# Performance work log

Measured on AMD Instinct MI355X. Metric: run time of the kernel, lower is better.

## Reference

```python
import jax, jax.numpy as jnp
import numpy as np

B, S, D, H = 2, 2048, 1024, 16
DK = D // H  # 64


def setup_inputs() -> dict:
    key = jax.random.key(0)
    ks = jax.random.split(key, 8)
    q = jax.random.normal(ks[0], (B, S, D), dtype=jnp.float32)
    k = jax.random.normal(ks[1], (B, S, D), dtype=jnp.float32)
    v = jax.random.normal(ks[2], (B, S, D), dtype=jnp.float32)
    mask = jax.random.randint(ks[3], (B, 1, S, S), 0, 2, dtype=jnp.int32)
    scale = 1.0 / np.sqrt(D)
    Wq = jax.random.normal(ks[4], (D, D), dtype=jnp.float32) * scale
    Wk = jax.random.normal(ks[5], (D, D), dtype=jnp.float32) * scale
    Wv = jax.random.normal(ks[6], (D, D), dtype=jnp.float32) * scale
    Wo = jax.random.normal(ks[7], (D, D), dtype=jnp.float32) * scale
    return {"q": q, "k": k, "v": v, "mask": mask,
            "Wq": Wq, "Wk": Wk, "Wv": Wv, "Wo": Wo}


def reference(q, k, v, mask, Wq, Wk, Wv, Wo):
    # Linear projections (torch nn.Linear: x @ W.T, no bias)
    qh = (q @ Wq.T).reshape(B, S, H, DK).transpose(0, 2, 1, 3)  # [B,H,S,DK]
    kh = (k @ Wk.T).reshape(B, S, H, DK).transpose(0, 2, 1, 3)
    vh = (v @ Wv.T).reshape(B, S, H, DK).transpose(0, 2, 1, 3)
    # Scaled dot-product attention with mask fill of -1e9 where mask == 0
    scores = jnp.einsum('bhqd,bhkd->bhqk', qh, kh) / jnp.sqrt(jnp.float32(DK))
    scores = jnp.where(mask == 0, jnp.float32(-1e9), scores)
    attn = jax.nn.softmax(scores, axis=-1)
    ctx = jnp.einsum('bhqk,bhkd->bhqd', attn, vh)  # [B,H,S,DK]
    ctx = ctx.transpose(0, 2, 1, 3).reshape(B, S, D)
    return ctx @ Wo.T
```

## Files before the change

### kernel.cpp

```cpp
#include <hip/hip_runtime.h>

using u16    = unsigned short;
using u32    = unsigned int;
using f32x4  = __attribute__((ext_vector_type(4))) float;
using f32x16 = __attribute__((ext_vector_type(16))) float;
using bf16x8 = __attribute__((ext_vector_type(8))) __bf16;
using u16x4  = __attribute__((ext_vector_type(4))) u16;
using u16x8  = __attribute__((ext_vector_type(8))) u16;
using u32x2  = __attribute__((ext_vector_type(2))) u32;
using u32x4  = __attribute__((ext_vector_type(4))) u32;
using i32x4  = __attribute__((ext_vector_type(4))) int;


__device__ __forceinline__ u16 f2bf(float f) {
  union { __bf16 b; u16 u; } c; c.b = (__bf16)f; return c.u;
}

typedef __attribute__((address_space(1))) const void GVoid;
typedef __attribute__((address_space(3))) void LVoid;

__device__ __forceinline__ void gload_lds16(const void* g, void* l) {
  __builtin_amdgcn_global_load_lds((GVoid*)g, (LVoid*)l, 16, 0, 0);
}

__global__ void cvt_w(const float* __restrict__ a, const float* __restrict__ b,
                      const float* __restrict__ c, const float* __restrict__ dd,
                      u16* __restrict__ oa, u16* __restrict__ ob,
                      u16* __restrict__ oc, u16* __restrict__ od) {
  int y = blockIdx.y;
  const float* s = (y == 0) ? a : (y == 1) ? b : (y == 2) ? c : dd;
  u16* d = (y == 0) ? oa : (y == 1) ? ob : (y == 2) ? oc : od;
  int i = blockIdx.x * 256 + threadIdx.x;
  f32x4 v = ((const f32x4*)s)[i];
  u16x4 r;
#pragma unroll
  for (int j = 0; j < 4; ++j) r[j] = f2bf(v[j]);
  ((u16x4*)d)[i] = r;
}

__global__ void pack_mask(const int* __restrict__ m, u32* __restrict__ mp) {
  int tid = blockIdx.x * 256 + threadIdx.x;
  int q = tid & 2047, kt = (tid >> 11) & 31, b = tid >> 16;
  const i32x4* src = (const i32x4*)(m + ((size_t)(b * 2048 + q)) * 2048 + kt * 64);
  u32 w0 = 0, w1 = 0;
#pragma unroll
  for (int j = 0; j < 8; ++j) {
    i32x4 a = src[j], c = src[j + 8];
#pragma unroll
    for (int e = 0; e < 4; ++e) {
      w0 |= (a[e] != 0 ? 1u : 0u) << (j * 4 + e);
      w1 |= (c[e] != 0 ? 1u : 0u) << (j * 4 + e);
    }
  }
  ((u32x2*)mp)[((size_t)(b * 32 + kt)) * 2048 + q] = u32x2{w0, w1};
}

__global__ __launch_bounds__(256, 2) void gemm_qkv(const float* __restrict__ Aq,
                                                   const float* __restrict__ Ak,
                                                   const float* __restrict__ Av,
                                                   const u16* __restrict__ Wb,
                                                   u16* __restrict__ out) {
  __shared__ alignas(16) char lds[32768];
  const int t = threadIdx.x;
  const int lane = t & 63, wid = t >> 6;
  const int g = lane >> 4, r16 = lane & 15;
  const int wm = wid >> 1, wn = wid & 1;
  const int m0 = blockIdx.x * 128, n0 = blockIdx.y * 128;
  const int z = blockIdx.z;

  const float* Axf = (z == 0) ? Aq : (z == 1) ? Ak : Av;
  const char* Ab = (const char*)Axf;
  const char* Bb = (const char*)(Wb + (size_t)z * 1048576);
  u16* op = out + (size_t)z * 4194304;
  const float qsc = (z == 0) ? 0.18033688011f : 1.0f;

  f32x4 acc[4][4] = {};

  for (int kk = 0; kk < 1024; kk += 64) {
#pragma unroll
    for (int i = 0; i < 4; ++i) {
      int ci = i * 256 + t;
      int row = ci >> 3;
      int cbs = ((ci & 7) << 4) ^ ((row & 7) << 4);
      gload_lds16(Bb + (size_t)(n0 + row) * 2048 + kk * 2 + cbs, lds + 16384 + ci * 16);
    }
#pragma unroll
    for (int i = 0; i < 4; ++i) {
      int ci = i * 256 + t;
      int row = ci >> 3;
      int cbs = ((ci & 7) << 4) ^ ((row & 7) << 4);
      const char* src = Ab + (size_t)(m0 + row) * 4096 + kk * 4 + cbs * 2;
      f32x4 a0 = *(const f32x4*)(src);
      f32x4 a1 = *(const f32x4*)(src + 16);
      u16x8 pk;
#pragma unroll
      for (int j = 0; j < 4; ++j) { pk[j] = f2bf(a0[j]); pk[4 + j] = f2bf(a1[j]); }
      *(u16x8*)(lds + ci * 16) = pk;
    }
    __syncthreads();
#pragma unroll
    for (int kc = 0; kc < 2; ++kc) {
      bf16x8 af[4], bfr[4];
#pragma unroll
      for (int mf = 0; mf < 4; ++mf) {
        int row = wm * 64 + mf * 16 + r16;
        af[mf] = *(const bf16x8*)(lds + row * 128 + ((64 * kc + 16 * g) ^ ((row & 7) << 4)));
      }
#pragma unroll
      for (int nf = 0; nf < 4; ++nf) {
        int row = wn * 64 + nf * 16 + r16;
        bfr[nf] = *(const bf16x8*)(lds + 16384 + row * 128 + ((64 * kc + 16 * g) ^ ((row & 7) << 4)));
      }
#pragma unroll
      for (int mf = 0; mf < 4; ++mf)
#pragma unroll
        for (int nf = 0; nf < 4; ++nf)
          acc[mf][nf] = __builtin_amdgcn_mfma_f32_16x16x32_bf16(af[mf], bfr[nf], acc[mf][nf], 0, 0, 0);
    }
    __syncthreads();
  }

#pragma unroll
  for (int mf = 0; mf < 4; ++mf) {
#pragma unroll
    for (int nf = 0; nf < 4; ++nf) {
      int mb = m0 + wm * 64 + mf * 16 + 4 * g;
      int n = n0 + wn * 64 + nf * 16 + r16;
      if (z == 0) {
        int bb = mb >> 11, h = n >> 6, dk = n & 63;
#pragma unroll
        for (int r = 0; r < 4; ++r) {
          int s = (mb + r) & 2047;
          op[((size_t)(bb * 16 + h) * 2048 + s) * 64 + dk] = f2bf(acc[mf][nf][r] * qsc);
        }
      } else if (z == 1) {
        int h = n >> 6, dk = n & 63;
#pragma unroll
        for (int r = 0; r < 4; ++r) {
          int m = mb + r;
          int bb = m >> 11, s = m & 2047;
          size_t off16 = ((((size_t)(bb * 16 + h) * 32 + (s >> 6)) * 2 + ((s >> 5) & 1)) * 8 +
                          (dk >> 3)) * 32 + (s & 31);
          op[off16 * 8 + (dk & 7)] = f2bf(acc[mf][nf][r]);
        }
      } else {
        int bb = mb >> 11, s = mb & 2047, h = n >> 6, d = n & 63;
        size_t off16 = ((((size_t)(bb * 16 + h) * 32 + (s >> 6)) * 8 + ((s & 63) >> 3)) * 2 +
                        (d >> 5)) * 32 + (d & 31);
        u16x4 pv;
#pragma unroll
        for (int r = 0; r < 4; ++r) pv[r] = f2bf(acc[mf][nf][r]);
        *(u16x4*)(op + off16 * 8 + (s & 7)) = pv;
      }
    }
  }
}

__global__ __launch_bounds__(256, 2) void gemm_out(const u16* __restrict__ X,
                                                   const u16* __restrict__ W,
                                                   float* __restrict__ out) {
  __shared__ alignas(16) char lds[32768];
  const int t = threadIdx.x;
  const int lane = t & 63, wid = t >> 6;
  const int g = lane >> 4, r16 = lane & 15;
  const int wm = wid >> 1, wn = wid & 1;
  const int m0 = blockIdx.x * 128, n0 = blockIdx.y * 128;
  const char* Ab = (const char*)X;
  const char* Bb = (const char*)W;

  f32x4 acc[4][4] = {};

  for (int kk = 0; kk < 1024; kk += 64) {
#pragma unroll
    for (int i = 0; i < 4; ++i) {
      int ci = i * 256 + t;
      int row = ci >> 3;
      int cbs = ((ci & 7) << 4) ^ ((row & 7) << 4);
      gload_lds16(Ab + (size_t)(m0 + row) * 2048 + kk * 2 + cbs, lds + ci * 16);
      gload_lds16(Bb + (size_t)(n0 + row) * 2048 + kk * 2 + cbs, lds + 16384 + ci * 16);
    }
    __syncthreads();
#pragma unroll
    for (int kc = 0; kc < 2; ++kc) {
      bf16x8 af[4], bfr[4];
#pragma unroll
      for (int mf = 0; mf < 4; ++mf) {
        int row = wm * 64 + mf * 16 + r16;
        af[mf] = *(const bf16x8*)(lds + row * 128 + ((64 * kc + 16 * g) ^ ((row & 7) << 4)));
      }
#pragma unroll
      for (int nf = 0; nf < 4; ++nf) {
        int row = wn * 64 + nf * 16 + r16;
        bfr[nf] = *(const bf16x8*)(lds + 16384 + row * 128 + ((64 * kc + 16 * g) ^ ((row & 7) << 4)));
      }
#pragma unroll
      for (int mf = 0; mf < 4; ++mf)
#pragma unroll
        for (int nf = 0; nf < 4; ++nf)
          acc[mf][nf] = __builtin_amdgcn_mfma_f32_16x16x32_bf16(af[mf], bfr[nf], acc[mf][nf], 0, 0, 0);
    }
    __syncthreads();
  }

#pragma unroll
  for (int mf = 0; mf < 4; ++mf)
#pragma unroll
    for (int nf = 0; nf < 4; ++nf) {
      int mb = m0 + wm * 64 + mf * 16 + 4 * g;
      int n = n0 + wn * 64 + nf * 16 + r16;
#pragma unroll
      for (int r = 0; r < 4; ++r) out[(size_t)(mb + r) * 1024 + n] = acc[mf][nf][r];
    }
}

struct KF { bf16x8 k0[4], k1[4]; };

__device__ __forceinline__ void loadK(KF& f, const char* p) {
#pragma unroll
  for (int c = 0; c < 4; ++c) {
    f.k0[c] = *(const bf16x8*)(p + c * 1024);
    f.k1[c] = *(const bf16x8*)(p + 4096 + c * 1024);
  }
}

__device__ __forceinline__ void attn_body(const bf16x8 (&qf)[4], KF& cur, KF& nxt,
                                          const char*& kp, const char*& vp0,
                                          const char*& vp1, const u32x2*& mptr,
                                          u32x2& mcur, int hi,
                                          f32x16& o0, f32x16& o1, float& l_run) {
  bf16x8 v0[4], v1[4];
#pragma unroll
  for (int ks = 0; ks < 4; ++ks) {
    v0[ks] = *(const bf16x8*)(vp0 + ks * 2048);
    v1[ks] = *(const bf16x8*)(vp1 + ks * 2048);
  }
  loadK(nxt, kp);
  u32x2 mnext = *mptr;
  kp += 8192; vp0 += 8192; vp1 += 8192; mptr += 2048;
  __builtin_amdgcn_sched_barrier(0);

  f32x16 s0 = {}, s1 = {};
#pragma unroll
  for (int c = 0; c < 4; ++c) {
    s0 = __builtin_amdgcn_mfma_f32_32x32x16_bf16(cur.k0[c], qf[c], s0, 0, 0, 0);
    s1 = __builtin_amdgcn_mfma_f32_32x32x16_bf16(cur.k1[c], qf[c], s1, 0, 0, 0);
  }

  u32 wa = mcur.x >> (4 * hi), wb = mcur.y >> (4 * hi);
  float ps = 0.f;
#pragma unroll
  for (int r = 0; r < 16; ++r) {
    const int bit = (r & 3) + 8 * (r >> 2);
    float p0 = __builtin_amdgcn_exp2f(s0[r]);
    float p1 = __builtin_amdgcn_exp2f(s1[r]);
    int sm0 = ((int)(wa << (31 - bit))) >> 31;
    int sm1 = ((int)(wb << (31 - bit))) >> 31;
    p0 = __uint_as_float(__float_as_uint(p0) & (u32)sm0);
    p1 = __uint_as_float(__float_as_uint(p1) & (u32)sm1);
    s0[r] = p0; s1[r] = p1;
    ps += p0 + p1;
  }
  l_run += ps;

  u32 w[16];
#pragma unroll
  for (int kb = 0; kb < 2; ++kb) {
#pragma unroll
    for (int ss = 0; ss < 2; ++ss) {
      const f32x16& sp = kb ? s1 : s0;
      u32 A0, B0, A1, B1;
      asm("v_cvt_pk_bf16_f32 %0, %1, %2" : "=v"(A0) : "v"(sp[8*ss+0]), "v"(sp[8*ss+1]));
      asm("v_cvt_pk_bf16_f32 %0, %1, %2" : "=v"(B0) : "v"(sp[8*ss+2]), "v"(sp[8*ss+3]));
      asm("v_cvt_pk_bf16_f32 %0, %1, %2" : "=v"(A1) : "v"(sp[8*ss+4]), "v"(sp[8*ss+5]));
      asm("v_cvt_pk_bf16_f32 %0, %1, %2" : "=v"(B1) : "v"(sp[8*ss+6]), "v"(sp[8*ss+7]));
      asm("v_permlane32_swap_b32 %0, %1" : "+v"(A0), "+v"(A1));
      asm("v_permlane32_swap_b32 %0, %1" : "+v"(B0), "+v"(B1));
      int f = 2 * kb + ss;
      w[4*f+0] = A0; w[4*f+1] = B0; w[4*f+2] = A1; w[4*f+3] = B1;
    }
  }

#pragma unroll
  for (int ks = 0; ks < 4; ++ks) {
    bf16x8 pa = __builtin_bit_cast(bf16x8, u32x4{w[4*ks], w[4*ks+1], w[4*ks+2], w[4*ks+3]});
    o0 = __builtin_amdgcn_mfma_f32_32x32x16_bf16(pa, v0[ks], o0, 0, 0, 0);
    o1 = __builtin_amdgcn_mfma_f32_32x32x16_bf16(pa, v1[ks], o1, 0, 0, 0);
  }
  mcur = mnext;
}

__global__ __launch_bounds__(256, 2) void attn_kern(const u16* __restrict__ Qh,
                                                    const u16* __restrict__ Kh,
                                                    const u16* __restrict__ Vt,
                                                    const u32* __restrict__ mp,
                                                    u16* __restrict__ ctx) {
  __shared__ float cmb[2][32][64];
  __shared__ float cmbl[2][64];
  const int t = threadIdx.x;
  const int wid = t >> 6, lane = t & 63;
  const int qw = wid & 1, kh = wid >> 1;
  const int hi = lane >> 5, l31 = lane & 31;

  const int wg = (blockIdx.x & 7) * 128 + (blockIdx.x >> 3);
  const int qt = wg & 31, bh = wg >> 5;
  const int b = bh >> 4, h = bh & 15;

  const char* qbytes = (const char*)Qh;
  const int qbase = qt * 64 + qw * 32;
  const int qg = qbase + l31;

  bf16x8 qf[4];
#pragma unroll
  for (int c = 0; c < 4; ++c)
    qf[c] = *(const bf16x8*)(qbytes + ((size_t)bh * 2048 + qg) * 128 + 32 * c + 16 * hi);

  const char* kp  = (const char*)Kh + (size_t)bh * 262144 + (size_t)kh * 131072 + hi * 512 + l31 * 16;
  const char* vp0 = (const char*)Vt + (size_t)bh * 262144 + (size_t)kh * 131072 + hi * 1024 + l31 * 16;
  const char* vp1 = vp0 + 512;
  const u32x2* mptr = (const u32x2*)mp + (size_t)b * 65536 + (size_t)kh * 32768 + qg;

  f32x16 o0 = {}, o1 = {};
  float l_run = 0.f;

  KF A, B2;
  loadK(A, kp);
  kp += 8192;
  u32x2 mcur = *mptr;
  mptr += 2048;

#pragma unroll 1
  for (int it = 0; it < 8; ++it) {
    attn_body(qf, A, B2, kp, vp0, vp1, mptr, mcur, hi, o0, o1, l_run);
    attn_body(qf, B2, A, kp, vp0, vp1, mptr, mcur, hi, o0, o1, l_run);
  }

  l_run += __shfl_xor(l_run, 32, 64);

  if (kh) {
#pragma unroll
    for (int r = 0; r < 16; ++r) {
      cmb[qw][r][lane]      = o0[r];
      cmb[qw][16 + r][lane] = o1[r];
    }
    cmbl[qw][lane] = l_run;
  }
  __syncthreads();
  if (!kh) {
#pragma unroll
    for (int r = 0; r < 16; ++r) {
      o0[r] += cmb[qw][r][lane];
      o1[r] += cmb[qw][16 + r][lane];
    }
    l_run += cmbl[qw][lane];

    float rl = 1.f / l_run;
#pragma unroll
    for (int r = 0; r < 16; ++r) {
      float rv = __shfl(rl, (r & 3) + 8 * (r >> 2) + 4 * hi, 64);
      int q = qbase + (r & 3) + 8 * (r >> 2) + 4 * hi;
      size_t rowp = ((size_t)b * 2048 + q) * 1024 + h * 64 + l31;
      ctx[rowp]      = f2bf(o0[r] * rv);
      ctx[rowp + 32] = f2bf(o1[r] * rv);
    }
  }
}

extern "C" void kernel_launch(void* const* d_in, const int* in_sizes, int n_in,
                              void* d_out, int out_size, void* d_ws, size_t ws_size,
                              hipStream_t stream) {
  const float* q  = (const float*)d_in[0];
  const float* k  = (const float*)d_in[1];
  const float* v  = (const float*)d_in[2];
  const int* mask = (const int*)d_in[3];
  const float* Wq = (const float*)d_in[4];
  const float* Wk = (const float*)d_in[5];
  const float* Wv = (const float*)d_in[6];
  const float* Wo = (const float*)d_in[7];

  u16* ws = (u16*)d_ws;
  const size_t NX = (size_t)4096 * 1024;
  const size_t NW = (size_t)1024 * 1024;
  u16* Wqb = ws + 3 * NX;
  u16* Qh  = Wqb + 4 * NW;
  u16* ctx = Qh + 3 * NX;
  u32* mpk = (u32*)ws;

  cvt_w<<<dim3(1024, 4), 256, 0, stream>>>(Wq, Wk, Wv, Wo,
                                           Wqb, Wqb + NW, Wqb + 2 * NW, Wqb + 3 * NW);
  pack_mask<<<dim3(512), 256, 0, stream>>>(mask, mpk);
  gemm_qkv<<<dim3(32, 8, 3), 256, 0, stream>>>(q, k, v, Wqb, Qh);
  attn_kern<<<dim3(1024), 256, 0, stream>>>(Qh, Qh + NX, Qh + 2 * NX, mpk, ctx);
  gemm_out<<<dim3(32, 8), 256, 0, stream>>>(ctx, Wqb + 3 * NW, (float*)d_out);
}
```

Measured before the change: 132.7 us.

## Prefetch next fp32 A tile into registers during QKV projection GEMM

The QKV projection GEMM now issues the fp32 activation loads for the next K-step into registers before the current step's MFMA work, using a two-buffer ping-pong loop unrolled by two. __syncthreads is replaced with explicit s_waitcnt vmcnt(8) plus raw s_barrier, so the prefetched loads stay in flight while the B tile's global_load_lds completes. The aim is to hide global-memory latency for the A operand. In exchange it uses more registers (32 extra f32x4), and the hand-counted vmcnt has to match the real number of outstanding loads.

```diff
diff --git a/kernel.cpp b/kernel.cpp
--- a/kernel.cpp
+++ b/kernel.cpp
@@ -76,7 +76,20 @@
 
   f32x4 acc[4][4] = {};
 
-  for (int kk = 0; kk < 1024; kk += 64) {
+  auto loadA = [&](f32x4 (&d0)[4], f32x4 (&d1)[4], int kk) {
+#pragma unroll
+    for (int i = 0; i < 4; ++i) {
+      int ci = i * 256 + t;
+      int row = ci >> 3;
+      int cbs = ((ci & 7) << 4) ^ ((row & 7) << 4);
+      const char* src = Ab + (size_t)(m0 + row) * 4096 + kk * 4 + cbs * 2;
+      d0[i] = *(const f32x4*)(src);
+      d1[i] = *(const f32x4*)(src + 16);
+    }
+  };
+
+  auto body = [&](int kk, f32x4 (&c0)[4], f32x4 (&c1)[4],
+                  f32x4 (&nn0)[4], f32x4 (&nn1)[4], bool pre) {
 #pragma unroll
     for (int i = 0; i < 4; ++i) {
       int ci = i * 256 + t;
@@ -87,17 +100,19 @@
 #pragma unroll
     for (int i = 0; i < 4; ++i) {
       int ci = i * 256 + t;
-      int row = ci >> 3;
-      int cbs = ((ci & 7) << 4) ^ ((row & 7) << 4);
-      const char* src = Ab + (size_t)(m0 + row) * 4096 + kk * 4 + cbs * 2;
-      f32x4 a0 = *(const f32x4*)(src);
-      f32x4 a1 = *(const f32x4*)(src + 16);
       u16x8 pk;
 #pragma unroll
-      for (int j = 0; j < 4; ++j) { pk[j] = f2bf(a0[j]); pk[4 + j] = f2bf(a1[j]); }
+      for (int j = 0; j < 4; ++j) { pk[j] = f2bf(c0[i][j]); pk[4 + j] = f2bf(c1[i][j]); }
       *(u16x8*)(lds + ci * 16) = pk;
     }
-    __syncthreads();
+    if (pre) {
+      loadA(nn0, nn1, kk + 64);
+      asm volatile("s_waitcnt vmcnt(8) lgkmcnt(0)" ::: "memory");
+    } else {
+      asm volatile("s_waitcnt vmcnt(0) lgkmcnt(0)" ::: "memory");
+    }
+    __builtin_amdgcn_s_barrier();
+    asm volatile("" ::: "memory");
 #pragma unroll
     for (int kc = 0; kc < 2; ++kc) {
       bf16x8 af[4], bfr[4];
@@ -117,7 +132,17 @@
         for (int nf = 0; nf < 4; ++nf)
           acc[mf][nf] = __builtin_amdgcn_mfma_f32_16x16x32_bf16(af[mf], bfr[nf], acc[mf][nf], 0, 0, 0);
     }
-    __syncthreads();
+    asm volatile("" ::: "memory");
+    __builtin_amdgcn_s_barrier();
+    asm volatile("" ::: "memory");
+  };
+
+  f32x4 A0[4], A1[4], N0[4], N1[4];
+  loadA(A0, A1, 0);
+#pragma unroll 1
+  for (int s = 0; s < 8; ++s) {
+    body(s * 128,      A0, A1, N0, N1, true);
+    body(s * 128 + 64, N0, N1, A0, A1, s < 7);
   }
 
 #pragma unroll
@@ -130,27 +155,27 @@
         int bb = mb >> 11, h = n >> 6, dk = n & 63;
 #pragma unroll
         for (int r = 0; r < 4; ++r) {
-          int s = (mb + r) & 2047;
-          op[((size_t)(bb * 16 + h) * 2048 + s) * 64 + dk] = f2bf(acc[mf][nf][r] * qsc);
+          int s2 = (mb + r) & 2047;
+          op[((size_t)(bb * 16 + h) * 2048 + s2) * 64 + dk] = f2bf(acc[mf][nf][r] * qsc);
         }
       } else if (z == 1) {
         int h = n >> 6, dk = n & 63;
 #pragma unroll
         for (int r = 0; r < 4; ++r) {
           int m = mb + r;
-          int bb = m >> 11, s = m & 2047;
-          size_t off16 = ((((size_t)(bb * 16 + h) * 32 + (s >> 6)) * 2 + ((s >> 5) & 1)) * 8 +
-                          (dk >> 3)) * 32 + (s & 31);
+          int bb = m >> 11, s2 = m & 2047;
+          size_t off16 = ((((size_t)(bb * 16 + h) * 32 + (s2 >> 6)) * 2 + ((s2 >> 5) & 1)) * 8 +
+                          (dk >> 3)) * 32 + (s2 & 31);
           op[off16 * 8 + (dk & 7)] = f2bf(acc[mf][nf][r]);
         }
       } else {
-        int bb = mb >> 11, s = mb & 2047, h = n >> 6, d = n & 63;
-        size_t off16 = ((((size_t)(bb * 16 + h) * 32 + (s >> 6)) * 8 + ((s & 63) >> 3)) * 2 +
+        int bb = mb >> 11, s2 = mb & 2047, h = n >> 6, d = n & 63;
+        size_t off16 = ((((size_t)(bb * 16 + h) * 32 + (s2 >> 6)) * 8 + ((s2 & 63) >> 3)) * 2 +
                         (d >> 5)) * 32 + (d & 31);
         u16x4 pv;
 #pragma unroll
         for (int r = 0; r < 4; ++r) pv[r] = f2bf(acc[mf][nf][r]);
-        *(u16x4*)(op + off16 * 8 + (s & 7)) = pv;
+        *(u16x4*)(op + off16 * 8 + (s2 & 7)) = pv;
       }
     }
   }
```

New measurement: 129.6 us. 1.02x faster.
